# Kernel optimization log

Measured on AMD Instinct MI355X. Metric: run time of the kernel, lower is better.

Reference implementation:

```python
import jax, jax.numpy as jnp
import numpy as np

B, H, W, C = 4, 64, 64, 512
DQK = C // 8


def setup_inputs() -> dict:
    key = jax.random.key(0)
    k1, k2, k3, k4 = jax.random.split(key, 4)
    x = jax.random.normal(k1, (B, H, W, C), dtype=jnp.float32)
    kernel_f = jax.random.normal(k2, (1, 1, C, DQK), dtype=jnp.float32) * 0.02
    kernel_g = jax.random.normal(k3, (1, 1, C, DQK), dtype=jnp.float32) * 0.02
    kernel_h = jax.random.normal(k4, (1, 1, C, C), dtype=jnp.float32) * 0.02
    gamma = jnp.ones((1,), dtype=jnp.float32)  # nonzero so attention branch contributes
    return {"x": x, "kernel_f": kernel_f, "kernel_g": kernel_g,
            "kernel_h": kernel_h, "gamma": gamma}


def reference(x, kernel_f, kernel_g, kernel_h, gamma):
    b, h, w, c = x.shape
    n = h * w
    xt = x.reshape(b, n, c)  # 1x1 conv == per-pixel matmul
    f = jnp.einsum('bnc,cd->bnd', xt, kernel_f[0, 0])       # [b,n,dqk]
    g = jnp.einsum('bnc,cd->bnd', xt, kernel_g[0, 0])       # [b,n,dqk]
    v = jnp.einsum('bnc,cd->bnd', xt, kernel_h[0, 0])       # [b,n,c]
    s = jnp.einsum('bid,bjd->bij', f, g)                    # [b,n,n] = f @ g^T
    beta = jax.nn.softmax(s, axis=-1)
    out = jnp.einsum('bij,bjc->bic', beta, v)               # [b,n,c]
    out = out.reshape(b, h, w, c)
    return gamma * out + x
```

## Files before the change

### kernel.cpp

```cpp
#include <hip/hip_runtime.h>


typedef __bf16 bf16x8 __attribute__((ext_vector_type(8)));
typedef __bf16 bf16x2 __attribute__((ext_vector_type(2)));
typedef float f32x4 __attribute__((ext_vector_type(4)));
typedef unsigned int u32x4 __attribute__((ext_vector_type(4)));
typedef unsigned int u32;

#define L2E 1.4426950408889634f

__device__ __forceinline__ unsigned short f2bf(float f) {
    unsigned int u = __builtin_bit_cast(unsigned int, f);
    u += 0x7fffu + ((u >> 16) & 1u);
    return (unsigned short)(u >> 16);
}
__device__ __forceinline__ u32 cvtpk(float a, float b) {
    bf16x2 t; t[0] = (__bf16)a; t[1] = (__bf16)b;
    return __builtin_bit_cast(u32, t);
}
__device__ __forceinline__ bf16x8 ld8(const void* p) {
    u32x4 u = *reinterpret_cast<const u32x4*>(p);
    return __builtin_bit_cast(bf16x8, u);
}
__device__ __forceinline__ bf16x8 ldx(const float* p) {
    float4 a = *reinterpret_cast<const float4*>(p);
    float4 b = *reinterpret_cast<const float4*>(p + 4);
    u32x4 r;
    r.x = cvtpk(a.x, a.y); r.y = cvtpk(a.z, a.w);
    r.z = cvtpk(b.x, b.y); r.w = cvtpk(b.z, b.w);
    return __builtin_bit_cast(bf16x8, r);
}
__device__ __forceinline__ f32x4 mfma16(bf16x8 a, bf16x8 b, f32x4 c) {
    return __builtin_amdgcn_mfma_f32_16x16x32_bf16(a, b, c, 0, 0, 0);
}
__device__ __forceinline__ void gl2lds16(const void* g, void* l) {
    __builtin_amdgcn_global_load_lds(
        (const __attribute__((address_space(1))) u32*)g,
        (__attribute__((address_space(3))) u32*)l, 16, 0, 0);
}

__global__ __launch_bounds__(256) void cvt_w_all(const float* __restrict__ kf,
                                                 const float* __restrict__ kg,
                                                 const float* __restrict__ kh,
                                                 unsigned short* __restrict__ wst) {
    int idx = blockIdx.x * 256 + threadIdx.x;
    int j = idx & 7;
    int gi = idx >> 3;
    int c = gi % 640;
    int sq = gi / 640;
    int k = (sq >> 2) * 32 + (sq & 3) * 8 + j;
    float v;
    if (c < 64)       v = kf[k * 64 + c] * L2E;
    else if (c < 128) v = kg[k * 64 + (c - 64)];
    else              v = kh[k * 512 + (c - 128)];
    wst[idx] = f2bf(v);
}

__global__ __launch_bounds__(256, 2) void proj_k(const float* __restrict__ x,
                                                 const unsigned short* __restrict__ wst,
                                                 unsigned short* __restrict__ fgb,
                                                 unsigned short* __restrict__ vt) {
    __shared__ __align__(16) unsigned char Wl[2][20480];
    __shared__ unsigned short Tl[64][72];

    int m0 = blockIdx.x * 64;
    int grp = blockIdx.y;
    int tid = threadIdx.x;
    int w = tid >> 6, l = tid & 63, g = l >> 4, i = l & 15;

    const char* wsrc = (const char*)wst + (size_t)w * 10240 + (size_t)grp * 5120 + l * 16;

#pragma unroll
    for (int s5 = 0; s5 < 5; s5++)
        gl2lds16(wsrc + s5 * 1024, &Wl[0][w * 5120 + s5 * 1024]);

    const float* xrow = x + (size_t)(m0 + 16 * w + i) * 512 + g * 8;
    bf16x8 af[16];
#pragma unroll
    for (int k = 0; k < 16; k++) af[k] = ldx(xrow + 32 * k);

    f32x4 acc[5][4];
#pragma unroll
    for (int t = 0; t < 5; t++)
#pragma unroll
        for (int cf = 0; cf < 4; cf++) acc[t][cf] = f32x4{0, 0, 0, 0};

    int rdoff = g * 5120 + i * 16;

#pragma unroll
    for (int q = 0; q < 16; q++) {
        __syncthreads();

        if (q < 15) {
            const char* src = wsrc + (size_t)(q + 1) * 40960;
#pragma unroll
            for (int s5 = 0; s5 < 5; s5++)
                gl2lds16(src + s5 * 1024, &Wl[(q + 1) & 1][w * 5120 + s5 * 1024]);
        }

        const unsigned char* Wb = &Wl[q & 1][0];
        __builtin_amdgcn_s_setprio(1);
#pragma unroll
        for (int t = 0; t < 5; t++)
#pragma unroll
            for (int cf = 0; cf < 4; cf++) {
                bf16x8 bb = ld8(Wb + rdoff + (t * 64 + 16 * cf) * 16);
                acc[t][cf] = mfma16(af[q], bb, acc[t][cf]);
            }
        __builtin_amdgcn_s_setprio(0);
    }

    int b = m0 >> 12, n = m0 & 4095;

#pragma unroll
    for (int t = 0; t < 5; t++) {
        bool isfg = (grp == 0) && (t < 2);
        if (isfg) {
#pragma unroll
            for (int cf = 0; cf < 4; cf++)
#pragma unroll
                for (int r = 0; r < 4; r++)
                    fgb[(size_t)(m0 + 16 * w + 4 * g + r) * 128 + t * 64 + 16 * cf + i] =
                        f2bf(acc[t][cf][r]);
        } else {
            int n0 = (grp == 0) ? (t - 2) * 64 : 192 + t * 64;
            __syncthreads();
#pragma unroll
            for (int cf = 0; cf < 4; cf++) {
                ushort4 v4;
                v4.x = f2bf(acc[t][cf][0]); v4.y = f2bf(acc[t][cf][1]);
                v4.z = f2bf(acc[t][cf][2]); v4.w = f2bf(acc[t][cf][3]);
                *reinterpret_cast<ushort4*>(&Tl[16 * cf + i][16 * w + 4 * g]) = v4;
            }
            __syncthreads();
#pragma unroll
            for (int ch = tid; ch < 1024; ch += 256) {
                int row = ch >> 4, nq = ch & 15;
                int w32 = nq >> 3, wq = nq & 7;
                int pos = w32 * 32 + (((wq & 3) << 1) + (wq >> 2)) * 4;
                ushort4 d = *reinterpret_cast<const ushort4*>(&Tl[row][nq * 4]);
                *reinterpret_cast<ushort4*>(vt + ((size_t)(b * 512 + n0 + row)) * 4096 + n + pos) = d;
            }
        }
    }
}

__global__ __launch_bounds__(256, 2) void attn_k(const unsigned short* __restrict__ fg,
                                                 const unsigned short* __restrict__ vt,
                                                 const float* __restrict__ x,
                                                 const float* __restrict__ gamma,
                                                 float* __restrict__ out) {
    __shared__ __align__(16) unsigned char Kl[2][8192];
    __shared__ __align__(16) unsigned char Vl[2][16384];

    int bid = blockIdx.x;
    int cs = bid & 3;
    int batch = (bid >> 2) & 3;
    int q = bid >> 4;
    int c0w = cs * 128;

    int tid = threadIdx.x;
    int w = tid >> 6, l = tid & 63, g = l >> 4, i = l & 15;
    int swz = (i & 7) << 4;
    int qbase = q * 128 + 32 * w;

    const unsigned short* fgb = fg + (size_t)batch * 4096 * 128;
    const char* vtB = (const char*)(vt + (size_t)batch * 512 * 4096);

    int kcol = (16 * (l & 7)) ^ (16 * (l >> 3));
    const char* kbase = (const char*)fgb + 128 + kcol + (size_t)(16 * w + (l >> 3)) * 256;
    const char* vbase = vtB + (size_t)(c0w + 32 * w + (l >> 3)) * 8192 + kcol;

    int koff0 = (16 * g) ^ swz, koff1 = (64 + 16 * g) ^ swz;

    bf16x8 aQ[2][2];
#pragma unroll
    for (int qf = 0; qf < 2; qf++)
#pragma unroll
        for (int ks = 0; ks < 2; ks++)
            aQ[qf][ks] = ld8(fgb + (size_t)(qbase + 16 * qf + i) * 128 + ks * 32 + g * 8);

    bf16x8 ones8;
#pragma unroll
    for (int z = 0; z < 8; z++) ones8[z] = (__bf16)1.0f;

    f32x4 acc[2][8];
#pragma unroll
    for (int a = 0; a < 2; a++)
#pragma unroll
        for (int b = 0; b < 8; b++) acc[a][b] = f32x4{0, 0, 0, 0};
    f32x4 lacc[2] = {f32x4{0,0,0,0}, f32x4{0,0,0,0}};

    {
        unsigned char* Kd = &Kl[0][w * 2048];
        gl2lds16(kbase, Kd);
        gl2lds16(kbase + 2048, Kd + 1024);
        unsigned char* Vd = &Vl[0][w * 4096];
        gl2lds16(vbase, Vd);
        gl2lds16(vbase + 65536, Vd + 1024);
        gl2lds16(vbase + 131072, Vd + 2048);
        gl2lds16(vbase + 196608, Vd + 3072);
    }

    int p = 0;
    for (int t = 0; t < 64; ++t) {
        __syncthreads();

        if (t + 1 < 64) {
            size_t j0n = (size_t)(t + 1) * 64;
            unsigned char* Kd = &Kl[p ^ 1][w * 2048];
            const char* gk = kbase + j0n * 256;
            gl2lds16(gk, Kd);
            gl2lds16(gk + 2048, Kd + 1024);
            unsigned char* Vd = &Vl[p ^ 1][w * 4096];
            const char* gv = vbase + j0n * 2;
            gl2lds16(gv, Vd);
            gl2lds16(gv + 65536, Vd + 1024);
            gl2lds16(gv + 131072, Vd + 2048);
            gl2lds16(gv + 196608, Vd + 3072);
        }

        const unsigned char* Kb = Kl[p];
        f32x4 sacc[4][2];
#pragma unroll
        for (int jf = 0; jf < 4; jf++)
#pragma unroll
            for (int qf = 0; qf < 2; qf++) sacc[jf][qf] = f32x4{0, 0, 0, 0};
        __builtin_amdgcn_s_setprio(1);
#pragma unroll
        for (int jf = 0; jf < 4; jf++) {
            const unsigned char* ra = Kb + (16 * jf + i) * 128;
            bf16x8 k0 = ld8(ra + koff0);
            bf16x8 k1 = ld8(ra + koff1);
            sacc[jf][0] = mfma16(k0, aQ[0][0], sacc[jf][0]);
            sacc[jf][1] = mfma16(k0, aQ[1][0], sacc[jf][1]);
            sacc[jf][0] = mfma16(k1, aQ[0][1], sacc[jf][0]);
            sacc[jf][1] = mfma16(k1, aQ[1][1], sacc[jf][1]);
        }
        __builtin_amdgcn_s_setprio(0);

        bf16x8 aP[2][2];
#pragma unroll
        for (int qf = 0; qf < 2; qf++) {
            u32 pk[4][2];
#pragma unroll
            for (int jf = 0; jf < 4; jf++) {
                float p0 = __builtin_amdgcn_exp2f(sacc[jf][qf][0]);
                float p1 = __builtin_amdgcn_exp2f(sacc[jf][qf][1]);
                float p2 = __builtin_amdgcn_exp2f(sacc[jf][qf][2]);
                float p3 = __builtin_amdgcn_exp2f(sacc[jf][qf][3]);
                pk[jf][0] = cvtpk(p0, p1);
                pk[jf][1] = cvtpk(p2, p3);
            }
            aP[qf][0] = __builtin_bit_cast(bf16x8, u32x4{pk[0][0], pk[0][1], pk[1][0], pk[1][1]});
            aP[qf][1] = __builtin_bit_cast(bf16x8, u32x4{pk[2][0], pk[2][1], pk[3][0], pk[3][1]});
        }

        const unsigned char* Vb = Vl[p];
        __builtin_amdgcn_s_setprio(1);
#pragma unroll
        for (int cf = 0; cf < 8; cf++) {
            const unsigned char* rv = Vb + (16 * cf + i) * 128;
            bf16x8 v0 = ld8(rv + koff0);
            bf16x8 v1 = ld8(rv + koff1);
            acc[0][cf] = mfma16(aP[0][0], v0, acc[0][cf]);
            acc[0][cf] = mfma16(aP[0][1], v1, acc[0][cf]);
            acc[1][cf] = mfma16(aP[1][0], v0, acc[1][cf]);
            acc[1][cf] = mfma16(aP[1][1], v1, acc[1][cf]);
        }
        lacc[0] = mfma16(aP[0][0], ones8, lacc[0]);
        lacc[0] = mfma16(aP[0][1], ones8, lacc[0]);
        lacc[1] = mfma16(aP[1][0], ones8, lacc[1]);
        lacc[1] = mfma16(aP[1][1], ones8, lacc[1]);
        __builtin_amdgcn_s_setprio(0);
        p ^= 1;
    }

    float gam = gamma[0];
#pragma unroll
    for (int qf = 0; qf < 2; qf++) {
#pragma unroll
        for (int r = 0; r < 4; r++) {
            float linv = gam / lacc[qf][r];
            int n = qbase + 16 * qf + 4 * g + r;
            size_t base = ((size_t)batch * 4096 + n) * 512 + c0w;
#pragma unroll
            for (int cf = 0; cf < 8; cf++)
                out[base + 16 * cf + i] = acc[qf][cf][r] * linv + x[base + 16 * cf + i];
        }
    }
}


extern "C" void kernel_launch(void* const* d_in, const int* in_sizes, int n_in,
                              void* d_out, int out_size, void* d_ws, size_t ws_size,
                              hipStream_t stream) {
    const float* x = (const float*)d_in[0];
    const float* kf = (const float*)d_in[1];
    const float* kg = (const float*)d_in[2];
    const float* kh = (const float*)d_in[3];
    const float* gamma = (const float*)d_in[4];
    float* out = (float*)d_out;

    char* ws = (char*)d_ws;
    unsigned short* FGb = (unsigned short*)(ws);
    unsigned short* Vt  = (unsigned short*)(ws + 4194304);
    unsigned short* Wst = (unsigned short*)(ws + 20971520);

    cvt_w_all<<<1280, 256, 0, stream>>>(kf, kg, kh, Wst);
    proj_k<<<dim3(256, 2), 256, 0, stream>>>(x, Wst, FGb, Vt);
    attn_k<<<512, 256, 0, stream>>>(FGb, Vt, x, gamma, out);
}
```

Measured before the change: 132.6 us.

## Double query rows per wave in attention kernel and remap blocks to XCDs

Each wave now handles 64 query rows instead of 32, so each K/V tile loaded into LDS feeds twice as much MFMA work. The grid is halved to 256 blocks, and occupancy drops to one block per CU to make room for the larger accumulators. Block IDs are also remapped so that each XCD (bid & 7) serves a single batch, which should improve L2 locality for K/V. The trade-off is higher register pressure and fewer resident waves to hide latency, plus only 256 blocks, fewer than one per CU.

```diff
diff --git a/kernel.cpp b/kernel.cpp
--- a/kernel.cpp
+++ b/kernel.cpp
@@ -145,7 +145,7 @@
     }
 }
 
-__global__ __launch_bounds__(256, 2) void attn_k(const unsigned short* __restrict__ fg,
+__global__ __launch_bounds__(256, 1) void attn_k(const unsigned short* __restrict__ fg,
                                                  const unsigned short* __restrict__ vt,
                                                  const float* __restrict__ x,
                                                  const float* __restrict__ gamma,
@@ -154,15 +154,17 @@
     __shared__ __align__(16) unsigned char Vl[2][16384];
 
     int bid = blockIdx.x;
-    int cs = bid & 3;
-    int batch = (bid >> 2) & 3;
-    int q = bid >> 4;
+    int xcd = bid & 7;
+    int batch = xcd >> 1;
+    int r = bid >> 3;
+    int cs = ((xcd & 1) << 1) | (r & 1);
+    int q = r >> 1;
     int c0w = cs * 128;
 
     int tid = threadIdx.x;
     int w = tid >> 6, l = tid & 63, g = l >> 4, i = l & 15;
     int swz = (i & 7) << 4;
-    int qbase = q * 128 + 32 * w;
+    int qbase = q * 256 + 64 * w;
 
     const unsigned short* fgb = fg + (size_t)batch * 4096 * 128;
     const char* vtB = (const char*)(vt + (size_t)batch * 512 * 4096);
@@ -173,9 +175,9 @@
 
     int koff0 = (16 * g) ^ swz, koff1 = (64 + 16 * g) ^ swz;
 
-    bf16x8 aQ[2][2];
-#pragma unroll
-    for (int qf = 0; qf < 2; qf++)
+    bf16x8 aQ[4][2];
+#pragma unroll
+    for (int qf = 0; qf < 4; qf++)
 #pragma unroll
         for (int ks = 0; ks < 2; ks++)
             aQ[qf][ks] = ld8(fgb + (size_t)(qbase + 16 * qf + i) * 128 + ks * 32 + g * 8);
@@ -184,12 +186,12 @@
 #pragma unroll
     for (int z = 0; z < 8; z++) ones8[z] = (__bf16)1.0f;
 
-    f32x4 acc[2][8];
-#pragma unroll
-    for (int a = 0; a < 2; a++)
+    f32x4 acc[4][8];
+#pragma unroll
+    for (int a = 0; a < 4; a++)
 #pragma unroll
         for (int b = 0; b < 8; b++) acc[a][b] = f32x4{0, 0, 0, 0};
-    f32x4 lacc[2] = {f32x4{0,0,0,0}, f32x4{0,0,0,0}};
+    f32x4 lacc[4] = {f32x4{0,0,0,0}, f32x4{0,0,0,0}, f32x4{0,0,0,0}, f32x4{0,0,0,0}};
 
     {
         unsigned char* Kd = &Kl[0][w * 2048];
@@ -221,27 +223,32 @@
         }
 
         const unsigned char* Kb = Kl[p];
-        f32x4 sacc[4][2];
-#pragma unroll
-        for (int jf = 0; jf < 4; jf++)
-#pragma unroll
-            for (int qf = 0; qf < 2; qf++) sacc[jf][qf] = f32x4{0, 0, 0, 0};
-        __builtin_amdgcn_s_setprio(1);
+        bf16x8 kreg[4][2];
 #pragma unroll
         for (int jf = 0; jf < 4; jf++) {
             const unsigned char* ra = Kb + (16 * jf + i) * 128;
-            bf16x8 k0 = ld8(ra + koff0);
-            bf16x8 k1 = ld8(ra + koff1);
-            sacc[jf][0] = mfma16(k0, aQ[0][0], sacc[jf][0]);
-            sacc[jf][1] = mfma16(k0, aQ[1][0], sacc[jf][1]);
-            sacc[jf][0] = mfma16(k1, aQ[0][1], sacc[jf][0]);
-            sacc[jf][1] = mfma16(k1, aQ[1][1], sacc[jf][1]);
-        }
+            kreg[jf][0] = ld8(ra + koff0);
+            kreg[jf][1] = ld8(ra + koff1);
+        }
+
+        f32x4 sacc[4][4];
+#pragma unroll
+        for (int jf = 0; jf < 4; jf++)
+#pragma unroll
+            for (int qf = 0; qf < 4; qf++) sacc[jf][qf] = f32x4{0, 0, 0, 0};
+        __builtin_amdgcn_s_setprio(1);
+#pragma unroll
+        for (int jf = 0; jf < 4; jf++)
+#pragma unroll
+            for (int qf = 0; qf < 4; qf++) {
+                sacc[jf][qf] = mfma16(kreg[jf][0], aQ[qf][0], sacc[jf][qf]);
+                sacc[jf][qf] = mfma16(kreg[jf][1], aQ[qf][1], sacc[jf][qf]);
+            }
         __builtin_amdgcn_s_setprio(0);
 
-        bf16x8 aP[2][2];
-#pragma unroll
-        for (int qf = 0; qf < 2; qf++) {
+        bf16x8 aP[4][2];
+#pragma unroll
+        for (int qf = 0; qf < 4; qf++) {
             u32 pk[4][2];
 #pragma unroll
             for (int jf = 0; jf < 4; jf++) {
@@ -263,30 +270,32 @@
             const unsigned char* rv = Vb + (16 * cf + i) * 128;
             bf16x8 v0 = ld8(rv + koff0);
             bf16x8 v1 = ld8(rv + koff1);
-            acc[0][cf] = mfma16(aP[0][0], v0, acc[0][cf]);
-            acc[0][cf] = mfma16(aP[0][1], v1, acc[0][cf]);
-            acc[1][cf] = mfma16(aP[1][0], v0, acc[1][cf]);
-            acc[1][cf] = mfma16(aP[1][1], v1, acc[1][cf]);
-        }
-        lacc[0] = mfma16(aP[0][0], ones8, lacc[0]);
-        lacc[0] = mfma16(aP[0][1], ones8, lacc[0]);
-        lacc[1] = mfma16(aP[1][0], ones8, lacc[1]);
-        lacc[1] = mfma16(aP[1][1], ones8, lacc[1]);
+#pragma unroll
+            for (int qf = 0; qf < 4; qf++) {
+                acc[qf][cf] = mfma16(aP[qf][0], v0, acc[qf][cf]);
+                acc[qf][cf] = mfma16(aP[qf][1], v1, acc[qf][cf]);
+            }
+        }
+#pragma unroll
+        for (int qf = 0; qf < 4; qf++) {
+            lacc[qf] = mfma16(aP[qf][0], ones8, lacc[qf]);
+            lacc[qf] = mfma16(aP[qf][1], ones8, lacc[qf]);
+        }
         __builtin_amdgcn_s_setprio(0);
         p ^= 1;
     }
 
     float gam = gamma[0];
 #pragma unroll
-    for (int qf = 0; qf < 2; qf++) {
-#pragma unroll
-        for (int r = 0; r < 4; r++) {
-            float linv = gam / lacc[qf][r];
-            int n = qbase + 16 * qf + 4 * g + r;
+    for (int qf = 0; qf < 4; qf++) {
+#pragma unroll
+        for (int r2 = 0; r2 < 4; r2++) {
+            float linv = gam / lacc[qf][r2];
+            int n = qbase + 16 * qf + 4 * g + r2;
             size_t base = ((size_t)batch * 4096 + n) * 512 + c0w;
 #pragma unroll
             for (int cf = 0; cf < 8; cf++)
-                out[base + 16 * cf + i] = acc[qf][cf][r] * linv + x[base + 16 * cf + i];
+                out[base + 16 * cf + i] = acc[qf][cf][r2] * linv + x[base + 16 * cf + i];
         }
     }
 }
@@ -309,5 +318,5 @@
 
     cvt_w_all<<<1280, 256, 0, stream>>>(kf, kg, kh, Wst);
     proj_k<<<dim3(256, 2), 256, 0, stream>>>(x, Wst, FGb, Vt);
-    attn_k<<<512, 256, 0, stream>>>(FGb, Vt, x, gamma, out);
-}
+    attn_k<<<256, 256, 0, stream>>>(FGb, Vt, x, gamma, out);
+}
```

After: 172.2 us. 1.3x slower.
